# Optimization experiments

Measured on AMD Instinct MI355X. Metric: run time of the kernel, lower is better.

The kernel has to match this reference:

```python
import jax, jax.numpy as jnp
import numpy as np

HIDDEN = 1024
INNER = 1024
LR = 0.01
EPS = 1e-5


def _layernorm(x, gamma, beta):
    mu = jnp.mean(x, axis=-1, keepdims=True)
    var = jnp.var(x, axis=-1, keepdims=True)
    return (x - mu) * jax.lax.rsqrt(var + EPS) * gamma + beta


def setup_inputs() -> dict:
    key = jax.random.key(0)
    ks = jax.random.split(key, 8)
    B, S, H, I = 64, 512, HIDDEN, INNER
    x = jax.random.normal(ks[0], (B, S, H), dtype=jnp.float32)
    W_init = jax.random.normal(ks[1], (H, I), dtype=jnp.float32) * 0.02
    b_init = jnp.zeros((I,), dtype=jnp.float32)
    # Linear weights stored as (in, out) so y = x @ W + b
    lim_t = 1.0 / np.sqrt(H)
    Wt = jax.random.uniform(ks[2], (H, I), jnp.float32, -lim_t, lim_t)
    bt = jnp.zeros((I,), dtype=jnp.float32)
    lim_o = 1.0 / np.sqrt(I)
    Wo = jax.random.uniform(ks[3], (I, H), jnp.float32, -lim_o, lim_o)
    bo = jnp.zeros((H,), dtype=jnp.float32)
    lim_g = 1.0 / np.sqrt(2 * H)
    Wg = jax.random.uniform(ks[4], (2 * H, H), jnp.float32, -lim_g, lim_g)
    bg = jnp.zeros((H,), dtype=jnp.float32)
    gamma = jnp.ones((H,), dtype=jnp.float32)
    beta = jnp.zeros((H,), dtype=jnp.float32)
    return {"x": x, "W_init": W_init, "b_init": b_init, "Wt": Wt, "bt": bt,
            "Wo": Wo, "bo": bo, "Wg": Wg, "bg": bg, "gamma": gamma, "beta": beta}


def reference(x, W_init, b_init, Wt, bt, Wo, bo, Wg, bg, gamma, beta):
    B, S, H = x.shape
    I = W_init.shape[1]
    W0 = jnp.broadcast_to(W_init[None], (B, H, I))  # per-batch fast weights
    b0 = jnp.broadcast_to(b_init[None], (B, I))

    def step(carry, x_t):
        W, b = carry
        inner = jnp.einsum('bh,bhi->bi', x_t, W) + b          # [B, I]
        ttt = jax.nn.silu(inner) @ Wo + bo                    # [B, H]
        g = jax.nn.sigmoid(jnp.concatenate([x_t, ttt], axis=-1) @ Wg + bg)
        out = _layernorm(g * ttt + (1.0 - g) * x_t, gamma, beta)
        # test-time training update (target detached)
        target = jax.lax.stop_gradient(x_t @ Wt + bt)
        err = inner - target                                   # [B, I]
        W = W - (LR / I) * x_t[:, :, None] * err[:, None, :]
        b = b - (LR / I) * err
        return (W, b), out

    xs = jnp.swapaxes(x, 0, 1)  # [S, B, H]
    (_, _), ys = jax.lax.scan(step, (W0, b0), xs)
    return jnp.swapaxes(ys, 0, 1)  # [B, S, H]
```

## Files before the change

kernel.cpp:

```cpp
#include <hip/hip_runtime.h>

#define HD 1024
#define ID 1024
#define BATCH 64
#define SEQ 512
#define BS (BATCH*SEQ)
#define CHUNK 64
#define NCHUNK (SEQ/CHUNK)
#define LR_OVER_I (0.01f/1024.0f)

typedef unsigned int u32;
typedef unsigned short ushort_t;
typedef __attribute__((ext_vector_type(8))) short short8;
typedef __attribute__((ext_vector_type(8))) unsigned short ushort8;
typedef __attribute__((ext_vector_type(4))) unsigned short ushort4v;
typedef __attribute__((ext_vector_type(4))) float floatx4;

__device__ inline ushort_t f2bf(float f) {
    union { float f; u32 u; } v; v.f = f;
    return (ushort_t)((v.u + 0x7FFFu + ((v.u >> 16) & 1u)) >> 16);
}
__device__ inline float bf2f(ushort_t h) {
    union { u32 u; float f; } v; v.u = ((u32)h) << 16; return v.f;
}

__device__ inline void load_lds16(const void* g, void* l) {
    __builtin_amdgcn_global_load_lds(
        (const __attribute__((address_space(1))) u32*)g,
        (__attribute__((address_space(3))) u32*)l, 16, 0, 0);
}

__global__ void prep_all(const float* __restrict__ x, ushort_t* __restrict__ xb,
                         const float* __restrict__ Wi, const float* __restrict__ Wt,
                         ushort_t* __restrict__ WdT, ushort_t* __restrict__ WtT,
                         const float* __restrict__ bi, const float* __restrict__ bt,
                         float* __restrict__ bd,
                         const float* __restrict__ Wo, const float* __restrict__ Wg,
                         ushort_t* __restrict__ WoT, ushort_t* __restrict__ WgT)
{
    __shared__ float t1[32][33], t2[32][33];
    int bid = blockIdx.x;
    const int tid = threadIdx.x;
    if (bid < 16384) {
        long i = ((long)bid * 256 + tid) * 8;
        float4 a = *(const float4*)(x + i);
        float4 b = *(const float4*)(x + i + 4);
        ushort8 o;
        o[0] = f2bf(a.x); o[1] = f2bf(a.y); o[2] = f2bf(a.z); o[3] = f2bf(a.w);
        o[4] = f2bf(b.x); o[5] = f2bf(b.y); o[6] = f2bf(b.z); o[7] = f2bf(b.w);
        *(ushort8*)(xb + i) = o;
        return;
    }
    bid -= 16384;
    const int tx = tid & 31, ty = tid >> 5;
    if (bid < 1024) {
        if (bid == 0)
            for (int i = tid; i < ID; i += 256) bd[i] = bi[i] - bt[i];
        int r0 = (bid >> 5) * 32, c0 = (bid & 31) * 32;
        for (int i = ty; i < 32; i += 8) {
            t1[i][tx] = Wi[(long)(r0 + i) * ID + c0 + tx];
            t2[i][tx] = Wt[(long)(r0 + i) * ID + c0 + tx];
        }
        __syncthreads();
        for (int i = ty; i < 32; i += 8) {
            float wi = t1[tx][i], wt = t2[tx][i];
            WdT[(long)(c0 + i) * HD + r0 + tx] = f2bf(wi - wt);
            WtT[(long)(c0 + i) * HD + r0 + tx] = f2bf(wt);
        }
        return;
    }
    bid -= 1024;
    int z = bid >> 10, tile = bid & 1023;
    const float* in; ushort_t* outp; int ldo;
    if (z == 0)      { in = Wo;                 outp = WoT;      ldo = ID; }
    else if (z == 1) { in = Wg;                 outp = WgT;      ldo = 2 * HD; }
    else             { in = Wg + (long)HD * HD; outp = WgT + HD; ldo = 2 * HD; }
    int r0 = (tile >> 5) * 32, c0 = (tile & 31) * 32;
    for (int i = ty; i < 32; i += 8)
        t1[i][tx] = in[(long)(r0 + i) * HD + c0 + tx];
    __syncthreads();
    for (int i = ty; i < 32; i += 8)
        outp[(long)(c0 + i) * ldo + r0 + tx] = f2bf(t1[tx][i]);
}

__global__ __launch_bounds__(256, 3) void gemm_bf16(
    const ushort_t* __restrict__ A0, long sA0, int lda0,
    const ushort_t* __restrict__ A1, long sA1, int lda1,
    const ushort_t* __restrict__ Bt, long sBb, int ldb,
    void* __restrict__ Cv, long sCb, int ldc,
    int KSEG, const float* __restrict__ bias,
    float alpha, float add0, int flags,
    const ushort_t* __restrict__ Bt2, void* __restrict__ Cv2,
    const float* __restrict__ bias2, int flags2)
{
    long zb = blockIdx.z;
    int fl = flags;
    if (flags & 16) {
        zb = 0;
        if (blockIdx.z == 1) { Bt = Bt2; Cv = Cv2; bias = bias2; fl = flags2; }
    }
    int bx, by;
    {
        int L = blockIdx.y * gridDim.x + blockIdx.x;
        if ((gridDim.y & 7) == 0) {
            int xcd = L & 7, g = L >> 3;
            bx = g % gridDim.x;
            by = (g / gridDim.x) * 8 + xcd;
        } else { bx = blockIdx.x; by = blockIdx.y; }
    }
    const int M0 = by * 128, N0 = bx * 128;
    if ((fl & 2) && N0 > M0) return;

    __shared__ ushort_t As[128 * 32];
    __shared__ ushort_t Bs[128 * 32];
    const int tid = threadIdx.x;
    const int wave = tid >> 6, lane = tid & 63;
    const int lr = lane & 15, lq = lane >> 4;
    const int wm = (wave & 1) * 64, wn = (wave >> 1) * 64;

    ushort_t* la0 = &As[(wave * 16)      * 32];
    ushort_t* la1 = &As[(wave * 16 + 64) * 32];
    ushort_t* lb0 = &Bs[(wave * 16)      * 32];
    ushort_t* lb1 = &Bs[(wave * 16 + 64) * 32];

    const ushort_t* gb0 = Bt + zb * sBb
                        + (long)(N0 + wave * 16 + (lane >> 2)) * ldb + (lane & 3) * 8;
    const ushort_t* gb1 = gb0 + 64L * ldb;

    floatx4 acc[4][4] = {};

    for (int seg = 0; seg < 2; ++seg) {
        const ushort_t* Ag = (seg == 0) ? A0 : A1;
        if (!Ag) break;
        const int lda = (seg == 0) ? lda0 : lda1;
        Ag += zb * ((seg == 0) ? sA0 : sA1);
        const ushort_t* ga0 = Ag + (long)(M0 + wave * 16 + (lane >> 2)) * lda + (lane & 3) * 8;
        const ushort_t* ga1 = ga0 + 64L * lda;

        for (int k0 = 0; k0 < KSEG; k0 += 32) {
            load_lds16(ga0, la0);
            load_lds16(ga1, la1);
            load_lds16(gb0, lb0);
            load_lds16(gb1, lb1);
            ga0 += 32; ga1 += 32; gb0 += 32; gb1 += 32;
            __syncthreads();
            short8 af[4], bf4[4];
#pragma unroll
            for (int i = 0; i < 4; ++i)
                af[i] = *(const short8*)&As[(wm + i * 16 + lr) * 32 + lq * 8];
#pragma unroll
            for (int j = 0; j < 4; ++j)
                bf4[j] = *(const short8*)&Bs[(wn + j * 16 + lr) * 32 + lq * 8];
#pragma unroll
            for (int i = 0; i < 4; ++i)
#pragma unroll
                for (int j = 0; j < 4; ++j)
                    acc[i][j] = __builtin_amdgcn_mfma_f32_16x16x32_bf16(
                        af[i], bf4[j], acc[i][j], 0, 0, 0);
            __syncthreads();
        }
    }

    float bv[4] = {0.f, 0.f, 0.f, 0.f};
    if (bias) {
#pragma unroll
        for (int j = 0; j < 4; ++j) bv[j] = bias[N0 + wn + j * 16 + lr];
    }
    if (fl & 1) {
        ushort_t* C = (ushort_t*)Cv + zb * sCb;
#pragma unroll
        for (int i = 0; i < 4; ++i)
#pragma unroll
            for (int r = 0; r < 4; ++r) {
                int row = M0 + wm + i * 16 + lq * 4 + r;
                ushort_t* cp = C + (long)row * ldc + N0 + wn + lr;
#pragma unroll
                for (int j = 0; j < 4; ++j)
                    cp[j * 16] = f2bf(alpha * acc[i][j][r] + add0 + bv[j]);
            }
    } else {
        if ((fl & 8) && wm) return;
        float* C = (float*)Cv + zb * sCb;
#pragma unroll
        for (int i = 0; i < 4; ++i)
#pragma unroll
            for (int r = 0; r < 4; ++r) {
                int row = M0 + wm + i * 16 + lq * 4 + r;
                float* cp = C + (long)row * ldc + N0 + wn + lr;
#pragma unroll
                for (int j = 0; j < 4; ++j) {
                    float val = alpha * acc[i][j][r] + add0 + bv[j];
                    if (fl & 4) val += cp[j * 16];
                    cp[j * 16] = val;
                }
            }
    }
}

__global__ __launch_bounds__(256) void solve_all(const float* __restrict__ u,
                                                 const ushort_t* __restrict__ gram,
                                                 ushort_t* __restrict__ ebt,
                                                 ushort_t* __restrict__ tgtb)
{
    const int b = blockIdx.z;
    const int j0 = blockIdx.x << 8;
    const int tid = threadIdx.x;
    const int wave = tid >> 6, lane = tid & 63;
    const int lr = lane & 15, lq = lane >> 4;

    __shared__ float Us[64][260];
    __shared__ __align__(16) char smem2[4096 + 16384];
    ushort_t* As = (ushort_t*)smem2;
    ushort_t* Bs = (ushort_t*)(smem2 + 4096);
    float* Gs = (float*)smem2;

    const ushort_t* Gbase = gram + (long)b * SEQ * SEQ;
    const float* Ubase = u + (long)b * SEQ * ID;
    ushort_t* Eb = ebt + (long)b * ID * SEQ;
    ushort_t* Tbase = tgtb + (long)b * SEQ * ID;

    for (int c = 0; c < NCHUNK; ++c) {
        const int t0 = c << 6;
        const ushort_t* Gb = Gbase + (long)t0 * SEQ;
        const float* Ub = Ubase + (long)t0 * ID;

        __syncthreads();

        if (c > 0) {
            const int K = c << 6;
            floatx4 acc[4][4] = {};
            const ushort_t* ga = Gb + (long)(wave * 16 + (lane >> 2)) * SEQ + (lane & 3) * 8;
            const ushort_t* gb = Eb + (long)(j0 + wave * 16 + (lane >> 2)) * SEQ + (lane & 3) * 8;
            ushort_t* la  = &As[(wave * 16) * 32];
            ushort_t* lb0 = &Bs[(wave * 16)       * 32];
            ushort_t* lb1 = &Bs[(64  + wave * 16) * 32];
            ushort_t* lb2 = &Bs[(128 + wave * 16) * 32];
            ushort_t* lb3 = &Bs[(192 + wave * 16) * 32];
            for (int k0 = 0; k0 < K; k0 += 32) {
                load_lds16(ga, la);
                load_lds16(gb,              lb0);
                load_lds16(gb + 64L * SEQ,  lb1);
                load_lds16(gb + 128L * SEQ, lb2);
                load_lds16(gb + 192L * SEQ, lb3);
                ga += 32; gb += 32;
                __syncthreads();
                short8 af[4], bf4[4];
#pragma unroll
                for (int i = 0; i < 4; ++i)
                    af[i] = *(const short8*)&As[(i * 16 + lr) * 32 + lq * 8];
#pragma unroll
                for (int j = 0; j < 4; ++j)
                    bf4[j] = *(const short8*)&Bs[(wave * 64 + j * 16 + lr) * 32 + lq * 8];
#pragma unroll
                for (int i = 0; i < 4; ++i)
#pragma unroll
                    for (int j = 0; j < 4; ++j)
                        acc[i][j] = __builtin_amdgcn_mfma_f32_16x16x32_bf16(
                            af[i], bf4[j], acc[i][j], 0, 0, 0);
                __syncthreads();
            }
#pragma unroll
            for (int i = 0; i < 4; ++i)
#pragma unroll
                for (int r = 0; r < 4; ++r) {
                    int row = i * 16 + lq * 4 + r;
                    const float* up = Ub + (long)row * ID + j0 + wave * 64 + lr;
#pragma unroll
                    for (int j = 0; j < 4; ++j)
                        Us[row][wave * 64 + j * 16 + lr] = up[j * 16] - acc[i][j][r];
                }
        } else {
            for (int idx = tid; idx < 64 * 64; idx += 256) {
                int row = idx >> 6, col4 = (idx & 63) << 2;
                float4 v = *(const float4*)(Ub + (long)row * ID + j0 + col4);
                Us[row][col4 + 0] = v.x; Us[row][col4 + 1] = v.y;
                Us[row][col4 + 2] = v.z; Us[row][col4 + 3] = v.w;
            }
        }

        for (int v = tid; v < 512; v += 256) {
            int row = v >> 3, col8 = (v & 7) << 3;
            ushort8 g8 = *(const ushort8*)(Gb + (long)row * SEQ + t0 + col8);
#pragma unroll
            for (int k = 0; k < 8; ++k) Gs[row * 64 + col8 + k] = bf2f(g8[k]);
        }
        __syncthreads();

        float e[64];
        e[0] = Us[0][tid];
#pragma unroll
        for (int t = 1; t < 64; ++t) {
            float v = Us[t][tid];
            float p0 = 0.f, p1 = 0.f, p2 = 0.f, p3 = 0.f;
#pragma unroll
            for (int s = 0; s + 3 < t; s += 4) {
                p0 = fmaf(Gs[t * 64 + s + 0], e[s + 0], p0);
                p1 = fmaf(Gs[t * 64 + s + 1], e[s + 1], p1);
                p2 = fmaf(Gs[t * 64 + s + 2], e[s + 2], p2);
                p3 = fmaf(Gs[t * 64 + s + 3], e[s + 3], p3);
            }
#pragma unroll
            for (int s = t & ~3; s < t; ++s)
                p0 = fmaf(Gs[t * 64 + s], e[s], p0);
            e[t] = v - ((p0 + p1) + (p2 + p3));
        }

        if (c < NCHUNK - 1) {
            ushort_t* EB = Eb + (long)(j0 + tid) * SEQ + t0;
#pragma unroll
            for (int g = 0; g < 8; ++g) {
                ushort8 o;
#pragma unroll
                for (int k = 0; k < 8; ++k) o[k] = f2bf(e[g * 8 + k]);
                *(ushort8*)(EB + g * 8) = o;
            }
        }

        ushort_t* Tp = Tbase + (long)t0 * ID + j0 + tid;
#pragma unroll
        for (int t = 0; t < 64; ++t) {
            float v = e[t] + bf2f(Tp[(long)t * ID]);
            Tp[(long)t * ID] = f2bf(v / (1.0f + __expf(-v)));
        }
    }
}

__global__ __launch_bounds__(256) void gate_ln(
    const ushort_t* __restrict__ zb, const ushort_t* __restrict__ tttb,
    const float* __restrict__ x, const float* __restrict__ gamma,
    const float* __restrict__ bet, float* __restrict__ out)
{
    long base = (long)blockIdx.x * HD + threadIdx.x * 4;
    ushort4v zv4 = *(const ushort4v*)(zb + base);
    ushort4v tv4 = *(const ushort4v*)(tttb + base);
    float4 xv = *(const float4*)(x + base);
    float xr[4] = {xv.x, xv.y, xv.z, xv.w};
    float y[4];
#pragma unroll
    for (int k = 0; k < 4; ++k) {
        float g = 1.0f / (1.0f + __expf(-bf2f(zv4[k])));
        float t = bf2f(tv4[k]);
        y[k] = g * t + (1.0f - g) * xr[k];
    }
    float sum = y[0] + y[1] + y[2] + y[3];
    float sq  = y[0]*y[0] + y[1]*y[1] + y[2]*y[2] + y[3]*y[3];
#pragma unroll
    for (int off = 32; off > 0; off >>= 1) {
        sum += __shfl_down(sum, off);
        sq  += __shfl_down(sq, off);
    }
    __shared__ float s1[4], s2[4];
    int wid = threadIdx.x >> 6;
    if ((threadIdx.x & 63) == 0) { s1[wid] = sum; s2[wid] = sq; }
    __syncthreads();
    float tot = s1[0] + s1[1] + s1[2] + s1[3];
    float tsq = s2[0] + s2[1] + s2[2] + s2[3];
    float mu = tot * (1.0f / HD);
    float var = tsq * (1.0f / HD) - mu * mu;
    float rs = rsqrtf(var + 1e-5f);
    int col = threadIdx.x * 4;
    float4 ov;
    ov.x = (y[0] - mu) * rs * gamma[col + 0] + bet[col + 0];
    ov.y = (y[1] - mu) * rs * gamma[col + 1] + bet[col + 1];
    ov.z = (y[2] - mu) * rs * gamma[col + 2] + bet[col + 2];
    ov.w = (y[3] - mu) * rs * gamma[col + 3] + bet[col + 3];
    *(float4*)(out + base) = ov;
}

extern "C" void kernel_launch(void* const* d_in, const int* in_sizes, int n_in,
                              void* d_out, int out_size, void* d_ws, size_t ws_size,
                              hipStream_t stream)
{
    const float* x    = (const float*)d_in[0];
    const float* Wi   = (const float*)d_in[1];
    const float* bi   = (const float*)d_in[2];
    const float* Wt   = (const float*)d_in[3];
    const float* bt   = (const float*)d_in[4];
    const float* Wo   = (const float*)d_in[5];
    const float* bo   = (const float*)d_in[6];
    const float* Wg   = (const float*)d_in[7];
    const float* bg   = (const float*)d_in[8];
    const float* gam  = (const float*)d_in[9];
    const float* bet  = (const float*)d_in[10];
    float* out = (float*)d_out;

    float* u       = (float*)d_ws;
    ushort_t* tgtb = (ushort_t*)(u + (long)BS * ID);
    float* gram    = (float*)(tgtb + (long)BS * ID);
    ushort_t* xb   = (ushort_t*)(gram + (long)BATCH * SEQ * SEQ);
    ushort_t* tttb = xb + (long)BS * HD;
    ushort_t* WdT  = tttb + (long)BS * HD;
    ushort_t* WtT  = WdT + (long)HD * ID;
    ushort_t* WoT  = WtT + (long)HD * ID;
    ushort_t* WgT  = WoT + (long)HD * ID;
    float* bd      = (float*)(WgT + (long)HD * 2 * HD);
    ushort_t* gramb = (ushort_t*)gram;
    ushort_t* ebt   = (ushort_t*)tttb;
    ushort_t* hb    = tgtb;
    ushort_t* zb    = (ushort_t*)u;

    prep_all<<<16384 + 1024 + 3072, 256, 0, stream>>>(
        x, xb, Wi, Wt, WdT, WtT, bi, bt, bd, Wo, Wg, WoT, WgT);

    dim3 gBig(ID / 128, BS / 128, 1);
    gemm_bf16<<<dim3(ID / 128, BS / 128, 2), 256, 0, stream>>>(
        xb, 0, HD, nullptr, 0, 0, WdT, 0, HD,
        u, 0, ID, HD, bd, 1.f, 0.f, 16,
        WtT, tgtb, bt, 1);
    gemm_bf16<<<dim3(SEQ / 128, SEQ / 128, BATCH), 256, 0, stream>>>(
        xb, (long)SEQ * HD, HD, nullptr, 0, 0, xb, (long)SEQ * HD, HD,
        gramb, (long)SEQ * SEQ, SEQ, HD, nullptr, LR_OVER_I, LR_OVER_I, 2 | 1,
        nullptr, nullptr, nullptr, 0);

    solve_all<<<dim3(4, 1, BATCH), 256, 0, stream>>>(u, gramb, ebt, tgtb);

    gemm_bf16<<<gBig, 256, 0, stream>>>(hb, 0, ID, nullptr, 0, 0, WoT, 0, ID,
                                        tttb, 0, HD, ID, bo, 1.f, 0.f, 1,
                                        nullptr, nullptr, nullptr, 0);
    gemm_bf16<<<gBig, 256, 0, stream>>>(xb, 0, HD, tttb, 0, HD, WgT, 0, 2 * HD,
                                        zb, 0, HD, HD, bg, 1.f, 0.f, 1,
                                        nullptr, nullptr, nullptr, 0);
    gate_ln<<<BS, 256, 0, stream>>>(zb, tttb, x, gam, bet, out);
}
```

Measured before the change: 1.225 ms.

## Split chunked solve into per-chunk launches with double-buffered LDS staging

The persistent per-batch solve kernel, which looped over all chunks, becomes one launch per chunk with the chunk index passed as an argument. The inner GEMM that corrects the chunk residual now double-buffers its LDS tiles: the next K-slice is staged while the current one is consumed, leaving one barrier per step instead of two. The residual tile is now loaded asynchronously straight into LDS and corrected in place. This trades a few extra kernel launches for less barrier stalling, more load/compute overlap and possibly lower register pressure per kernel.

```diff
diff --git a/kernel.cpp b/kernel.cpp
--- a/kernel.cpp
+++ b/kernel.cpp
@@ -197,131 +197,128 @@
     }
 }
 
-__global__ __launch_bounds__(256) void solve_all(const float* __restrict__ u,
-                                                 const ushort_t* __restrict__ gram,
-                                                 ushort_t* __restrict__ ebt,
-                                                 ushort_t* __restrict__ tgtb)
+__global__ __launch_bounds__(256) void solve_chunk(const float* __restrict__ u,
+                                                   const ushort_t* __restrict__ gram,
+                                                   ushort_t* __restrict__ ebt,
+                                                   ushort_t* __restrict__ tgtb, int c)
 {
     const int b = blockIdx.z;
     const int j0 = blockIdx.x << 8;
+    const int t0 = c << 6;
     const int tid = threadIdx.x;
     const int wave = tid >> 6, lane = tid & 63;
     const int lr = lane & 15, lq = lane >> 4;
 
     __shared__ float Us[64][260];
-    __shared__ __align__(16) char smem2[4096 + 16384];
-    ushort_t* As = (ushort_t*)smem2;
-    ushort_t* Bs = (ushort_t*)(smem2 + 4096);
+    __shared__ __align__(16) char smem2[2][20480];
     float* Gs = (float*)smem2;
 
-    const ushort_t* Gbase = gram + (long)b * SEQ * SEQ;
-    const float* Ubase = u + (long)b * SEQ * ID;
+    const ushort_t* Gb = gram + (long)b * SEQ * SEQ + (long)t0 * SEQ;
+    const float* Ub = u + (long)b * SEQ * ID + (long)t0 * ID;
     ushort_t* Eb = ebt + (long)b * ID * SEQ;
-    ushort_t* Tbase = tgtb + (long)b * SEQ * ID;
-
-    for (int c = 0; c < NCHUNK; ++c) {
-        const int t0 = c << 6;
-        const ushort_t* Gb = Gbase + (long)t0 * SEQ;
-        const float* Ub = Ubase + (long)t0 * ID;
-
+
+    {
+        const int r0w = wave * 16;
+#pragma unroll
+        for (int r = 0; r < 16; ++r)
+            load_lds16(Ub + (long)(r0w + r) * ID + j0 + (lane << 2), &Us[r0w + r][0]);
+    }
+
+    if (c > 0) {
+        const int K = c << 6;
+        floatx4 acc[4][4] = {};
+        const int arow = wave * 16 + (lane >> 2);
+        const int acol = (lane & 3) * 8;
+
+        auto stage = [&](int bsel, int k0) {
+            ushort_t* As_ = (ushort_t*)smem2[bsel];
+            ushort_t* Bs_ = (ushort_t*)(smem2[bsel] + 4096);
+            const ushort_t* ga = Gb + (long)arow * SEQ + acol + k0;
+            const ushort_t* gb = Eb + (long)(j0 + arow) * SEQ + acol + k0;
+            load_lds16(ga,               &As_[(wave * 16) * 32]);
+            load_lds16(gb,               &Bs_[(wave * 16)       * 32]);
+            load_lds16(gb + 64L * SEQ,   &Bs_[(64  + wave * 16) * 32]);
+            load_lds16(gb + 128L * SEQ,  &Bs_[(128 + wave * 16) * 32]);
+            load_lds16(gb + 192L * SEQ,  &Bs_[(192 + wave * 16) * 32]);
+        };
+
+        stage(0, 0);
         __syncthreads();
-
-        if (c > 0) {
-            const int K = c << 6;
-            floatx4 acc[4][4] = {};
-            const ushort_t* ga = Gb + (long)(wave * 16 + (lane >> 2)) * SEQ + (lane & 3) * 8;
-            const ushort_t* gb = Eb + (long)(j0 + wave * 16 + (lane >> 2)) * SEQ + (lane & 3) * 8;
-            ushort_t* la  = &As[(wave * 16) * 32];
-            ushort_t* lb0 = &Bs[(wave * 16)       * 32];
-            ushort_t* lb1 = &Bs[(64  + wave * 16) * 32];
-            ushort_t* lb2 = &Bs[(128 + wave * 16) * 32];
-            ushort_t* lb3 = &Bs[(192 + wave * 16) * 32];
-            for (int k0 = 0; k0 < K; k0 += 32) {
-                load_lds16(ga, la);
-                load_lds16(gb,              lb0);
-                load_lds16(gb + 64L * SEQ,  lb1);
-                load_lds16(gb + 128L * SEQ, lb2);
-                load_lds16(gb + 192L * SEQ, lb3);
-                ga += 32; gb += 32;
-                __syncthreads();
-                short8 af[4], bf4[4];
-#pragma unroll
-                for (int i = 0; i < 4; ++i)
-                    af[i] = *(const short8*)&As[(i * 16 + lr) * 32 + lq * 8];
+        int buf = 0;
+        for (int k0 = 0; k0 < K; k0 += 32) {
+            if (k0 + 32 < K) stage(buf ^ 1, k0 + 32);
+            const ushort_t* As_ = (const ushort_t*)smem2[buf];
+            const ushort_t* Bs_ = (const ushort_t*)(smem2[buf] + 4096);
+            short8 af[4], bf4[4];
+#pragma unroll
+            for (int i = 0; i < 4; ++i)
+                af[i] = *(const short8*)&As_[(i * 16 + lr) * 32 + lq * 8];
+#pragma unroll
+            for (int j = 0; j < 4; ++j)
+                bf4[j] = *(const short8*)&Bs_[(wave * 64 + j * 16 + lr) * 32 + lq * 8];
+#pragma unroll
+            for (int i = 0; i < 4; ++i)
 #pragma unroll
                 for (int j = 0; j < 4; ++j)
-                    bf4[j] = *(const short8*)&Bs[(wave * 64 + j * 16 + lr) * 32 + lq * 8];
-#pragma unroll
-                for (int i = 0; i < 4; ++i)
-#pragma unroll
-                    for (int j = 0; j < 4; ++j)
-                        acc[i][j] = __builtin_amdgcn_mfma_f32_16x16x32_bf16(
-                            af[i], bf4[j], acc[i][j], 0, 0, 0);
-                __syncthreads();
+                    acc[i][j] = __builtin_amdgcn_mfma_f32_16x16x32_bf16(
+                        af[i], bf4[j], acc[i][j], 0, 0, 0);
+            __syncthreads();
+            buf ^= 1;
+        }
+#pragma unroll
+        for (int i = 0; i < 4; ++i)
+#pragma unroll
+            for (int r = 0; r < 4; ++r) {
+                int row = i * 16 + lq * 4 + r;
+#pragma unroll
+                for (int j = 0; j < 4; ++j)
+                    Us[row][wave * 64 + j * 16 + lr] -= acc[i][j][r];
             }
-#pragma unroll
-            for (int i = 0; i < 4; ++i)
-#pragma unroll
-                for (int r = 0; r < 4; ++r) {
-                    int row = i * 16 + lq * 4 + r;
-                    const float* up = Ub + (long)row * ID + j0 + wave * 64 + lr;
-#pragma unroll
-                    for (int j = 0; j < 4; ++j)
-                        Us[row][wave * 64 + j * 16 + lr] = up[j * 16] - acc[i][j][r];
-                }
-        } else {
-            for (int idx = tid; idx < 64 * 64; idx += 256) {
-                int row = idx >> 6, col4 = (idx & 63) << 2;
-                float4 v = *(const float4*)(Ub + (long)row * ID + j0 + col4);
-                Us[row][col4 + 0] = v.x; Us[row][col4 + 1] = v.y;
-                Us[row][col4 + 2] = v.z; Us[row][col4 + 3] = v.w;
-            }
-        }
-
-        for (int v = tid; v < 512; v += 256) {
-            int row = v >> 3, col8 = (v & 7) << 3;
-            ushort8 g8 = *(const ushort8*)(Gb + (long)row * SEQ + t0 + col8);
-#pragma unroll
-            for (int k = 0; k < 8; ++k) Gs[row * 64 + col8 + k] = bf2f(g8[k]);
-        }
-        __syncthreads();
-
-        float e[64];
-        e[0] = Us[0][tid];
-#pragma unroll
-        for (int t = 1; t < 64; ++t) {
-            float v = Us[t][tid];
-            float p0 = 0.f, p1 = 0.f, p2 = 0.f, p3 = 0.f;
-#pragma unroll
-            for (int s = 0; s + 3 < t; s += 4) {
-                p0 = fmaf(Gs[t * 64 + s + 0], e[s + 0], p0);
-                p1 = fmaf(Gs[t * 64 + s + 1], e[s + 1], p1);
-                p2 = fmaf(Gs[t * 64 + s + 2], e[s + 2], p2);
-                p3 = fmaf(Gs[t * 64 + s + 3], e[s + 3], p3);
-            }
-#pragma unroll
-            for (int s = t & ~3; s < t; ++s)
-                p0 = fmaf(Gs[t * 64 + s], e[s], p0);
-            e[t] = v - ((p0 + p1) + (p2 + p3));
-        }
-
-        if (c < NCHUNK - 1) {
-            ushort_t* EB = Eb + (long)(j0 + tid) * SEQ + t0;
-#pragma unroll
-            for (int g = 0; g < 8; ++g) {
-                ushort8 o;
-#pragma unroll
-                for (int k = 0; k < 8; ++k) o[k] = f2bf(e[g * 8 + k]);
-                *(ushort8*)(EB + g * 8) = o;
-            }
-        }
-
-        ushort_t* Tp = Tbase + (long)t0 * ID + j0 + tid;
-#pragma unroll
-        for (int t = 0; t < 64; ++t) {
-            float v = e[t] + bf2f(Tp[(long)t * ID]);
-            Tp[(long)t * ID] = f2bf(v / (1.0f + __expf(-v)));
-        }
+    }
+
+    for (int v = tid; v < 512; v += 256) {
+        int row = v >> 3, col8 = (v & 7) << 3;
+        ushort8 g8 = *(const ushort8*)(Gb + (long)row * SEQ + t0 + col8);
+#pragma unroll
+        for (int k = 0; k < 8; ++k) Gs[row * 64 + col8 + k] = bf2f(g8[k]);
+    }
+    __syncthreads();
+
+    float e[64];
+    e[0] = Us[0][tid];
+#pragma unroll
+    for (int t = 1; t < 64; ++t) {
+        float v = Us[t][tid];
+        float p0 = 0.f, p1 = 0.f, p2 = 0.f, p3 = 0.f;
+#pragma unroll
+        for (int s = 0; s + 3 < t; s += 4) {
+            p0 = fmaf(Gs[t * 64 + s + 0], e[s + 0], p0);
+            p1 = fmaf(Gs[t * 64 + s + 1], e[s + 1], p1);
+            p2 = fmaf(Gs[t * 64 + s + 2], e[s + 2], p2);
+            p3 = fmaf(Gs[t * 64 + s + 3], e[s + 3], p3);
+        }
+#pragma unroll
+        for (int s = t & ~3; s < t; ++s)
+            p0 = fmaf(Gs[t * 64 + s], e[s], p0);
+        e[t] = v - ((p0 + p1) + (p2 + p3));
+    }
+
+    if (c < NCHUNK - 1) {
+        ushort_t* EB = Eb + (long)(j0 + tid) * SEQ + t0;
+#pragma unroll
+        for (int g = 0; g < 8; ++g) {
+            ushort8 o;
+#pragma unroll
+            for (int k = 0; k < 8; ++k) o[k] = f2bf(e[g * 8 + k]);
+            *(ushort8*)(EB + g * 8) = o;
+        }
+    }
+
+    ushort_t* Tp = tgtb + ((long)b * SEQ + t0) * ID + j0 + tid;
+#pragma unroll
+    for (int t = 0; t < 64; ++t) {
+        float v = e[t] + bf2f(Tp[(long)t * ID]);
+        Tp[(long)t * ID] = f2bf(v / (1.0f + __expf(-v)));
     }
 }
 
@@ -412,7 +409,8 @@
         gramb, (long)SEQ * SEQ, SEQ, HD, nullptr, LR_OVER_I, LR_OVER_I, 2 | 1,
         nullptr, nullptr, nullptr, 0);
 
-    solve_all<<<dim3(4, 1, BATCH), 256, 0, stream>>>(u, gramb, ebt, tgtb);
+    for (int c = 0; c < NCHUNK; ++c)
+        solve_chunk<<<dim3(4, 1, BATCH), 256, 0, stream>>>(u, gramb, ebt, tgtb, c);
 
     gemm_bf16<<<gBig, 256, 0, stream>>>(hb, 0, ID, nullptr, 0, 0, WoT, 0, ID,
                                         tttb, 0, HD, ID, bo, 1.f, 0.f, 1,
```

New measurement: 1.047 ms. 14.6% less time.
